# Optimization experiments

Hardware: AMD Instinct MI355X
Metric: run time of the kernel (lower is better)

The kernel has to match this reference:

```python
import jax, jax.numpy as jnp
import numpy as np

N_NODES = 100000
N_EDGES = 1600000
IN_FEATS = 128
N_HIDDEN = 128
N_CLASSES = 47


def _glorot(key, shape):
    fan_in, fan_out = shape
    lim = jnp.sqrt(6.0 / (fan_in + fan_out))
    return jax.random.uniform(key, shape, jnp.float32, -lim, lim)


def setup_inputs() -> dict:
    key = jax.random.key(0)
    ks = jax.random.split(key, 12)
    x = jax.random.normal(ks[0], (N_NODES, IN_FEATS), jnp.float32)
    src = jax.random.randint(ks[1], (N_EDGES,), 0, N_NODES, jnp.int32)
    dst = jax.random.randint(ks[2], (N_EDGES,), 0, N_NODES, jnp.int32)
    dims = [(IN_FEATS, N_HIDDEN), (N_HIDDEN, N_HIDDEN), (N_HIDDEN, N_CLASSES)]
    params = {}
    for l, (di, do) in enumerate(dims):
        params[f"Ws{l}"] = _glorot(ks[3 + 3 * l], (di, do))
        params[f"Wn{l}"] = _glorot(ks[4 + 3 * l], (di, do))
        params[f"b{l}"] = jnp.zeros((do,), jnp.float32)
    return {"x": x, "src": src, "dst": dst, **params}


def _sage_layer(h, src, dst, Ws, Wn, b):
    # mean aggregation over incoming edges (irregular gather + segment-reduce)
    n = h.shape[0]
    msg = h[src]  # [E, F]
    agg = jax.ops.segment_sum(msg, dst, num_segments=n)
    deg = jax.ops.segment_sum(jnp.ones((src.shape[0],), h.dtype), dst, num_segments=n)
    agg = agg / jnp.maximum(deg, 1.0)[:, None]
    return h @ Ws + agg @ Wn + b


def reference(x, src, dst, Ws0, Wn0, b0, Ws1, Wn1, b1, Ws2, Wn2, b2):
    layers = [(Ws0, Wn0, b0), (Ws1, Wn1, b1), (Ws2, Wn2, b2)]
    h = x
    for l, (Ws, Wn, b) in enumerate(layers):
        h = _sage_layer(h, src, dst, Ws, Wn, b)
        if l != len(layers) - 1:
            h = jax.nn.relu(h)  # dropout is identity at inference
    return h
```

## Files before the change

kernel.cpp:

```cpp
#include <hip/hip_runtime.h>
#include <cstdint>
#include <cstddef>

static const int NN = 100000;
static const int NE = 1600000;
static const int F  = 128;
static const int BKT_SHIFT = 9;
static const int BNODES = 1 << BKT_SHIFT;
static const int NBKT = (NN + BNODES - 1) >> BKT_SHIFT;
static const int SRC_BITS = 17;
static const unsigned SRC_MASK = (1u << SRC_BITS) - 1u;

typedef __attribute__((ext_vector_type(8))) short short8;
typedef __attribute__((ext_vector_type(4))) float float4v;
typedef __attribute__((ext_vector_type(2))) float f32x2;

static __device__ __forceinline__ unsigned short f2bf(float f){
    unsigned u = __builtin_bit_cast(unsigned, f);
    unsigned r = (u + 0x7FFFu + ((u >> 16) & 1u)) >> 16;
    return (unsigned short)r;
}
static __device__ __forceinline__ float bf_lo(unsigned u){
    return __builtin_bit_cast(float, u << 16);
}
static __device__ __forceinline__ float bf_hi(unsigned u){
    return __builtin_bit_cast(float, u & 0xFFFF0000u);
}


__global__ __launch_bounds__(256) void bhist_k(const int* __restrict__ dst,
                                               int* __restrict__ bcnt, int E){
    __shared__ int h[NBKT];
    const int t = threadIdx.x;
    for (int i = t; i < NBKT; i += 256) h[i] = 0;
    __syncthreads();
    const int e0 = blockIdx.x * 2048;
    #pragma unroll
    for (int j = 0; j < 8; ++j){
        int e = e0 + j*256 + t;
        if (e < E) atomicAdd(&h[dst[e] >> BKT_SHIFT], 1);
    }
    __syncthreads();
    for (int i = t; i < NBKT; i += 256)
        if (h[i]) atomicAdd(&bcnt[i], h[i]);
}

__global__ __launch_bounds__(256) void bscan_k(const int* __restrict__ bcnt,
                                               int* __restrict__ bptr){
    __shared__ int sm[256];
    int t = threadIdx.x;
    int v = (t < NBKT) ? bcnt[t] : 0;
    sm[t] = v; __syncthreads();
    for (int off = 1; off < 256; off <<= 1){
        int add = (t >= off) ? sm[t-off] : 0;
        __syncthreads();
        sm[t] += add;
        __syncthreads();
    }
    if (t < NBKT) bptr[t+1] = sm[t];
    if (t == 0)   bptr[0] = 0;
}

__global__ __launch_bounds__(256) void bscatter_k(
        const int* __restrict__ src, const int* __restrict__ dst,
        const int* __restrict__ bptr, int* __restrict__ bfill,
        unsigned* __restrict__ pk, int E){
    __shared__ int hist[NBKT];
    __shared__ int gbase[NBKT];
    const int t = threadIdx.x;
    for (int i = t; i < NBKT; i += 256) hist[i] = 0;
    __syncthreads();
    const int e0 = blockIdx.x * 2048;
    int s[8], d[8], b[8], r[8];
    #pragma unroll
    for (int j = 0; j < 8; ++j){
        int e = e0 + j*256 + t;
        if (e < E){
            s[j] = src[e]; d[j] = dst[e];
            b[j] = d[j] >> BKT_SHIFT;
            r[j] = atomicAdd(&hist[b[j]], 1);
        }
    }
    __syncthreads();
    for (int i = t; i < NBKT; i += 256){
        int h = hist[i];
        int base = 0;
        if (h) base = atomicAdd(&bfill[i], h);
        gbase[i] = bptr[i] + base;
    }
    __syncthreads();
    #pragma unroll
    for (int j = 0; j < 8; ++j){
        int e = e0 + j*256 + t;
        if (e < E)
            pk[gbase[b[j]] + r[j]] =
                (unsigned)s[j] | ((unsigned)(d[j] & (BNODES-1)) << SRC_BITS);
    }
}

__global__ __launch_bounds__(1024) void sort_k(
        const unsigned* __restrict__ pk, const int* __restrict__ bptr,
        int* __restrict__ row_ptr, int* __restrict__ ssorted, int N, int E){
    __shared__ int hc[BNODES];
    __shared__ int of[BNODES];
    __shared__ int fi[BNODES];
    const int b  = blockIdx.x;
    const int n0 = b << BKT_SHIFT;
    const int t  = threadIdx.x;
    const int rbeg = bptr[b];
    const int rend = bptr[b+1];
    if (t < BNODES){ hc[t] = 0; fi[t] = 0; }
    __syncthreads();
    for (int e = rbeg + t; e < rend; e += 1024)
        atomicAdd(&hc[pk[e] >> SRC_BITS], 1);
    __syncthreads();
    if (t < BNODES) of[t] = hc[t];
    __syncthreads();
    for (int off = 1; off < BNODES; off <<= 1){
        int add = (t < BNODES && t >= off) ? of[t-off] : 0;
        __syncthreads();
        if (t < BNODES) of[t] += add;
        __syncthreads();
    }
    if (t < BNODES){
        int excl = of[t] - hc[t];
        of[t] = excl;
        int node = n0 + t;
        if (node <= N) row_ptr[node] = rbeg + excl;
    }
    __syncthreads();
    for (int e = rbeg + t; e < rend; e += 1024){
        unsigned p = pk[e];
        int dl = (int)(p >> SRC_BITS);
        int pos = rbeg + of[dl] + atomicAdd(&fi[dl], 1);
        ssorted[pos] = (int)(p & SRC_MASK);
    }
}


__global__ void xconv_k(const float* __restrict__ x, unsigned short* __restrict__ xb, int n4){
    int i = blockIdx.x*256 + threadIdx.x;
    if (i < n4){
        const float4* p = (const float4*)x + i;
        float4 v = *p;
        unsigned short o0 = f2bf(v.x), o1 = f2bf(v.y), o2 = f2bf(v.z), o3 = f2bf(v.w);
        ((unsigned*)xb)[i*2]   = (unsigned)o0 | ((unsigned)o1 << 16);
        ((unsigned*)xb)[i*2+1] = (unsigned)o2 | ((unsigned)o3 << 16);
    }
}

__global__ void prepw_all_k(const float* __restrict__ Ws0, const float* __restrict__ Wn0,
                            const float* __restrict__ Ws1, const float* __restrict__ Wn1,
                            const float* __restrict__ Ws2, const float* __restrict__ Wn2,
                            unsigned short* __restrict__ Wt0, unsigned short* __restrict__ Wt1,
                            unsigned short* __restrict__ Wt2){
    int i = blockIdx.x*256 + threadIdx.x;
    const float* Ws; const float* Wn; unsigned short* Wt; int D; int idx;
    if (i < 32768){       Ws=Ws0; Wn=Wn0; Wt=Wt0; D=128; idx=i; }
    else if (i < 65536){  Ws=Ws1; Wn=Wn1; Wt=Wt1; D=128; idx=i-32768; }
    else {                Ws=Ws2; Wn=Wn2; Wt=Wt2; D=47;  idx=i-65536; }
    int n = idx >> 7, k = idx & 127;
    float v = 0.f;
    if (n < D)        v = Ws[k*D + n];
    else if (n < 2*D) v = Wn[k*D + (n - D)];
    Wt[n*128 + k] = f2bf(v);
}


__global__ __launch_bounds__(256) void gemm_mfma_k(
        const unsigned short* __restrict__ hb,
        const unsigned short* __restrict__ Wt,
        const float* __restrict__ bias,
        unsigned short* __restrict__ Y,
        unsigned short* __restrict__ Z,
        int M, int D, int Dpad){
    __shared__ char ldsA[128*256];
    const int t = threadIdx.x;
    const int lane = t & 63;
    const int w = t >> 6;
    const int wm = w >> 1, wn = w & 1;
    const int tile = blockIdx.x * 128;
    const int cbase = blockIdx.y * 128;

    #pragma unroll
    for (int i = 0; i < 8; ++i){
        int chunkid = i*4 + w;
        int lin = chunkid*64 + lane;
        int row = lin >> 4;
        int cs  = lin & 15;
        int grow = tile + row; if (grow >= M) grow = M - 1;
        const char* src = (const char*)hb + (size_t)grow*256 + ((size_t)(cs ^ (row & 7)) << 4);
        __builtin_amdgcn_global_load_lds(
            (const __attribute__((address_space(1))) void*)src,
            (__attribute__((address_space(3))) void*)(ldsA + (size_t)chunkid*1024 + (size_t)lane*16),
            16, 0, 0);
    }

    short8 bfrag[4][4];
    {
        int ncol = cbase + wn*64;
        #pragma unroll
        for (int n = 0; n < 4; ++n){
            int wrow = ncol + n*16 + (lane & 15);
            const unsigned short* bp = Wt + (size_t)wrow*128 + ((lane >> 4) * 8);
            #pragma unroll
            for (int kk = 0; kk < 4; ++kk)
                bfrag[n][kk] = *(const short8*)(bp + kk*32);
        }
    }

    float4v acc[4][4];
    #pragma unroll
    for (int m = 0; m < 4; ++m)
        #pragma unroll
        for (int n = 0; n < 4; ++n)
            acc[m][n] = (float4v){0.f,0.f,0.f,0.f};

    __syncthreads();

    #pragma unroll
    for (int m = 0; m < 4; ++m){
        int r = wm*64 + m*16 + (lane & 15);
        #pragma unroll
        for (int kk = 0; kk < 4; ++kk){
            int c = kk*4 + (lane >> 4);
            short8 a = *(const short8*)(ldsA + (size_t)r*256 + ((size_t)(c ^ (r & 7)) << 4));
            #pragma unroll
            for (int n = 0; n < 4; ++n)
                acc[m][n] = __builtin_amdgcn_mfma_f32_16x16x32_bf16(a, bfrag[n][kk], acc[m][n], 0, 0, 0);
        }
    }

    #pragma unroll
    for (int m = 0; m < 4; ++m){
        #pragma unroll
        for (int n = 0; n < 4; ++n){
            int c = cbase + wn*64 + n*16 + (lane & 15);
            #pragma unroll
            for (int j = 0; j < 4; ++j){
                int r = tile + wm*64 + m*16 + (lane >> 4)*4 + j;
                if (r < M){
                    float v = acc[m][n][j];
                    if (c < D){
                        v += bias[c];
                        Y[(size_t)r*Dpad + c] = f2bf(v);
                    } else if (c < 2*D){
                        Z[(size_t)r*Dpad + (c - D)] = f2bf(v);
                    }
                }
            }
        }
    }
}


__global__ __launch_bounds__(256) void agg128_k(
        const unsigned short* __restrict__ Yb, const unsigned short* __restrict__ Zb,
        const int* __restrict__ row_ptr, const int* __restrict__ ssorted,
        unsigned short* __restrict__ hout, int N){
    const int lane = threadIdx.x & 63;
    const int q   = lane >> 4;
    const int sub = lane & 15;
    const int node = blockIdx.x*4 + (threadIdx.x >> 6);
    if (node >= N) return;
    const int beg = __builtin_amdgcn_readfirstlane(row_ptr[node]);
    const int end = __builtin_amdgcn_readfirstlane(row_ptr[node+1]);
    const float inv = 1.0f / fmaxf((float)(end - beg), 1.0f);
    const char* zc = (const char*)Zb;
    const unsigned boff = (unsigned)(sub*16);
    f32x2 a0={0.f,0.f}, a1={0.f,0.f}, a2={0.f,0.f}, a3={0.f,0.f};
    for (int e = beg; e < end; e += 32){
        int s[8];
        #pragma unroll
        for (int j = 0; j < 8; ++j){
            int ei = e + 4*j + q;
            int ec = ei < end ? ei : end - 1;
            s[j] = ssorted[ec];
        }
        uint4 u[8];
        #pragma unroll
        for (int j = 0; j < 8; ++j)
            u[j] = *(const uint4*)(zc + ((unsigned)s[j]*256u + boff));
        #pragma unroll
        for (int j = 0; j < 8; ++j){
            if (e + 4*j + q < end){
                a0 += (f32x2){ bf_lo(u[j].x), bf_hi(u[j].x) };
                a1 += (f32x2){ bf_lo(u[j].y), bf_hi(u[j].y) };
                a2 += (f32x2){ bf_lo(u[j].z), bf_hi(u[j].z) };
                a3 += (f32x2){ bf_lo(u[j].w), bf_hi(u[j].w) };
            }
        }
    }
    a0.x += __shfl_xor(a0.x,16,64); a0.x += __shfl_xor(a0.x,32,64);
    a0.y += __shfl_xor(a0.y,16,64); a0.y += __shfl_xor(a0.y,32,64);
    a1.x += __shfl_xor(a1.x,16,64); a1.x += __shfl_xor(a1.x,32,64);
    a1.y += __shfl_xor(a1.y,16,64); a1.y += __shfl_xor(a1.y,32,64);
    a2.x += __shfl_xor(a2.x,16,64); a2.x += __shfl_xor(a2.x,32,64);
    a2.y += __shfl_xor(a2.y,16,64); a2.y += __shfl_xor(a2.y,32,64);
    a3.x += __shfl_xor(a3.x,16,64); a3.x += __shfl_xor(a3.x,32,64);
    a3.y += __shfl_xor(a3.y,16,64); a3.y += __shfl_xor(a3.y,32,64);
    if (q == 0){
        uint4 yu = *(const uint4*)((const char*)Yb + (size_t)node*256 + sub*16);
        float r0 = fmaxf(bf_lo(yu.x) + a0.x*inv, 0.f);
        float r1 = fmaxf(bf_hi(yu.x) + a0.y*inv, 0.f);
        float r2 = fmaxf(bf_lo(yu.y) + a1.x*inv, 0.f);
        float r3 = fmaxf(bf_hi(yu.y) + a1.y*inv, 0.f);
        float r4 = fmaxf(bf_lo(yu.z) + a2.x*inv, 0.f);
        float r5 = fmaxf(bf_hi(yu.z) + a2.y*inv, 0.f);
        float r6 = fmaxf(bf_lo(yu.w) + a3.x*inv, 0.f);
        float r7 = fmaxf(bf_hi(yu.w) + a3.y*inv, 0.f);
        uint4 o;
        o.x = (unsigned)f2bf(r0) | ((unsigned)f2bf(r1) << 16);
        o.y = (unsigned)f2bf(r2) | ((unsigned)f2bf(r3) << 16);
        o.z = (unsigned)f2bf(r4) | ((unsigned)f2bf(r5) << 16);
        o.w = (unsigned)f2bf(r6) | ((unsigned)f2bf(r7) << 16);
        *(uint4*)((char*)hout + (size_t)node*256 + sub*16) = o;
    }
}

__global__ __launch_bounds__(256) void aggfin_k(
        const unsigned short* __restrict__ Yb, const unsigned short* __restrict__ Zb,
        const int* __restrict__ row_ptr, const int* __restrict__ ssorted,
        float* __restrict__ out, int N){
    const int lane = threadIdx.x & 63;
    const int q   = lane >> 4;
    const int sub = lane & 15;
    const int node = blockIdx.x*4 + (threadIdx.x >> 6);
    if (node >= N) return;
    const int beg = __builtin_amdgcn_readfirstlane(row_ptr[node]);
    const int end = __builtin_amdgcn_readfirstlane(row_ptr[node+1]);
    const float inv = 1.0f / fmaxf((float)(end - beg), 1.0f);
    const char* zc = (const char*)Zb;
    const bool act = (sub < 12);
    const unsigned boff = (unsigned)(sub*8);
    f32x2 acc0 = {0.f,0.f}, acc1 = {0.f,0.f};
    for (int e = beg; e < end; e += 32){
        int s[8];
        #pragma unroll
        for (int j = 0; j < 8; ++j){
            int ei = e + 4*j + q;
            int ec = ei < end ? ei : end - 1;
            s[j] = ssorted[ec];
        }
        #pragma unroll
        for (int j = 0; j < 8; ++j){
            if (act){
                uint2 u = *(const uint2*)(zc + ((unsigned)s[j]*96u + boff));
                if (e + 4*j + q < end){
                    acc0 += (f32x2){ bf_lo(u.x), bf_lo(u.y) };
                    acc1 += (f32x2){ bf_hi(u.x), bf_hi(u.y) };
                }
            }
        }
    }
    acc0.x += __shfl_xor(acc0.x, 16, 64); acc0.x += __shfl_xor(acc0.x, 32, 64);
    acc0.y += __shfl_xor(acc0.y, 16, 64); acc0.y += __shfl_xor(acc0.y, 32, 64);
    acc1.x += __shfl_xor(acc1.x, 16, 64); acc1.x += __shfl_xor(acc1.x, 32, 64);
    acc1.y += __shfl_xor(acc1.y, 16, 64); acc1.y += __shfl_xor(acc1.y, 32, 64);
    if (q == 0 && act){
        uint2 yu = *(const uint2*)((const char*)Yb + (size_t)node*96 + sub*8);
        float r0 = bf_lo(yu.x) + acc0.x*inv;
        float r1 = bf_hi(yu.x) + acc1.x*inv;
        float r2 = bf_lo(yu.y) + acc0.y*inv;
        float r3 = bf_hi(yu.y) + acc1.y*inv;
        int f = 4*sub;
        size_t o = (size_t)node*47 + f;
        out[o]   = r0;
        out[o+1] = r1;
        out[o+2] = r2;
        if (f + 3 < 47) out[o+3] = r3;
    }
}


extern "C" void kernel_launch(void* const* d_in, const int* in_sizes, int n_in,
                              void* d_out, int out_size, void* d_ws, size_t ws_size,
                              hipStream_t stream){
    const float* x   = (const float*)d_in[0];
    const int*   src = (const int*)  d_in[1];
    const int*   dstv= (const int*)  d_in[2];
    const float* Ws0 = (const float*)d_in[3];
    const float* Wn0 = (const float*)d_in[4];
    const float* b0  = (const float*)d_in[5];
    const float* Ws1 = (const float*)d_in[6];
    const float* Wn1 = (const float*)d_in[7];
    const float* b1  = (const float*)d_in[8];
    const float* Ws2 = (const float*)d_in[9];
    const float* Wn2 = (const float*)d_in[10];
    const float* b2  = (const float*)d_in[11];
    float* out = (float*)d_out;
    const int N = NN, E = NE;

    char* w = (char*)d_ws;
    size_t off = 0;
    auto alloc = [&](size_t bytes)->char*{
        char* p = w + off; off += (bytes + 255) & ~(size_t)255; return p;
    };
    int*   bbuf    = (int*)  alloc((size_t)(2*NBKT)*4);
    int*   bcnt    = bbuf;
    int*   bfill   = bbuf + NBKT;
    int*   bptr    = (int*)  alloc((size_t)(NBKT+1)*4);
    int*   row_ptr = (int*)  alloc((size_t)(NN+1)*4);
    int*   ssorted = (int*)  alloc((size_t)E*4);
    unsigned* pk   = (unsigned*)alloc((size_t)E*4);
    unsigned short* xb  = (unsigned short*)alloc((size_t)NN*F*2);
    unsigned short* hA  = (unsigned short*)alloc((size_t)NN*F*2);
    unsigned short* hB  = (unsigned short*)alloc((size_t)NN*F*2);
    unsigned short* Yb  = (unsigned short*)alloc((size_t)NN*F*2);
    unsigned short* Zb  = (unsigned short*)alloc((size_t)NN*F*2);
    unsigned short* Wt0 = (unsigned short*)alloc((size_t)256*128*2);
    unsigned short* Wt1 = (unsigned short*)alloc((size_t)256*128*2);
    unsigned short* Wt2 = (unsigned short*)alloc((size_t)128*128*2);
    (void)ws_size; (void)n_in; (void)in_sizes; (void)out_size;

    const int GE = (E + 2047)/2048;

    hipMemsetAsync(bbuf, 0, (size_t)(2*NBKT)*4, stream);
    bhist_k   <<<GE, 256, 0, stream>>>(dstv, bcnt, E);
    bscan_k   <<<1, 256, 0, stream>>>(bcnt, bptr);
    bscatter_k<<<GE, 256, 0, stream>>>(src, dstv, bptr, bfill, pk, E);
    sort_k    <<<NBKT, 1024, 0, stream>>>(pk, bptr, row_ptr, ssorted, N, E);

    xconv_k<<<(N*F/4 + 255)/256, 256, 0, stream>>>(x, xb, N*F/4);
    prepw_all_k<<<320, 256, 0, stream>>>(Ws0, Wn0, Ws1, Wn1, Ws2, Wn2, Wt0, Wt1, Wt2);

    const int GM = (N + 127)/128;
    const int GA = (N + 3)/4;

    gemm_mfma_k<<<dim3(GM,2), 256, 0, stream>>>(xb, Wt0, b0, Yb, Zb, N, 128, 128);
    agg128_k   <<<GA, 256, 0, stream>>>(Yb, Zb, row_ptr, ssorted, hA, N);
    gemm_mfma_k<<<dim3(GM,2), 256, 0, stream>>>(hA, Wt1, b1, Yb, Zb, N, 128, 128);
    agg128_k   <<<GA, 256, 0, stream>>>(Yb, Zb, row_ptr, ssorted, hB, N);
    gemm_mfma_k<<<dim3(GM,1), 256, 0, stream>>>(hB, Wt2, b2, Yb, Zb, N, 47, 48);
    aggfin_k   <<<GA, 256, 0, stream>>>(Yb, Zb, row_ptr, ssorted, out, N);
}
```

Baseline: 388.7 us.

## Drop bucket histogram pass with fixed-capacity buckets; cache edge indices in aggregation

Removes the bucket-count histogram and scan kernels by giving each destination bucket a fixed-capacity slot region (PKCAP) in the packed array. sort_k now recomputes bucket offsets from the fill counters with an in-block scan. The aggregation kernels preload up to 64 source indices per wave and spread them with shuffles instead of reloading them each iteration, and xconv now handles 8 floats per thread. The fixed capacity assumes no bucket gets more than 16384 edges (about 8192 expected for this input), so a skewed dst distribution would overflow silently.

```diff
diff --git a/kernel.cpp b/kernel.cpp
--- a/kernel.cpp
+++ b/kernel.cpp
@@ -8,6 +8,7 @@
 static const int BKT_SHIFT = 9;
 static const int BNODES = 1 << BKT_SHIFT;
 static const int NBKT = (NN + BNODES - 1) >> BKT_SHIFT;
+static const int PKCAP = 16384;
 static const int SRC_BITS = 17;
 static const unsigned SRC_MASK = (1u << SRC_BITS) - 1u;
 
@@ -15,10 +16,9 @@
 typedef __attribute__((ext_vector_type(4))) float float4v;
 typedef __attribute__((ext_vector_type(2))) float f32x2;
 
-static __device__ __forceinline__ unsigned short f2bf(float f){
+static __device__ __forceinline__ unsigned f2bf(float f){
     unsigned u = __builtin_bit_cast(unsigned, f);
-    unsigned r = (u + 0x7FFFu + ((u >> 16) & 1u)) >> 16;
-    return (unsigned short)r;
+    return (u + 0x7FFFu + ((u >> 16) & 1u)) >> 16;
 }
 static __device__ __forceinline__ float bf_lo(unsigned u){
     return __builtin_bit_cast(float, u << 16);
@@ -27,44 +27,9 @@
     return __builtin_bit_cast(float, u & 0xFFFF0000u);
 }
 
-
-__global__ __launch_bounds__(256) void bhist_k(const int* __restrict__ dst,
-                                               int* __restrict__ bcnt, int E){
-    __shared__ int h[NBKT];
-    const int t = threadIdx.x;
-    for (int i = t; i < NBKT; i += 256) h[i] = 0;
-    __syncthreads();
-    const int e0 = blockIdx.x * 2048;
-    #pragma unroll
-    for (int j = 0; j < 8; ++j){
-        int e = e0 + j*256 + t;
-        if (e < E) atomicAdd(&h[dst[e] >> BKT_SHIFT], 1);
-    }
-    __syncthreads();
-    for (int i = t; i < NBKT; i += 256)
-        if (h[i]) atomicAdd(&bcnt[i], h[i]);
-}
-
-__global__ __launch_bounds__(256) void bscan_k(const int* __restrict__ bcnt,
-                                               int* __restrict__ bptr){
-    __shared__ int sm[256];
-    int t = threadIdx.x;
-    int v = (t < NBKT) ? bcnt[t] : 0;
-    sm[t] = v; __syncthreads();
-    for (int off = 1; off < 256; off <<= 1){
-        int add = (t >= off) ? sm[t-off] : 0;
-        __syncthreads();
-        sm[t] += add;
-        __syncthreads();
-    }
-    if (t < NBKT) bptr[t+1] = sm[t];
-    if (t == 0)   bptr[0] = 0;
-}
-
 __global__ __launch_bounds__(256) void bscatter_k(
         const int* __restrict__ src, const int* __restrict__ dst,
-        const int* __restrict__ bptr, int* __restrict__ bfill,
-        unsigned* __restrict__ pk, int E){
+        int* __restrict__ bfill, unsigned* __restrict__ pk, int E){
     __shared__ int hist[NBKT];
     __shared__ int gbase[NBKT];
     const int t = threadIdx.x;
@@ -86,7 +51,7 @@
         int h = hist[i];
         int base = 0;
         if (h) base = atomicAdd(&bfill[i], h);
-        gbase[i] = bptr[i] + base;
+        gbase[i] = i*PKCAP + base;
     }
     __syncthreads();
     #pragma unroll
@@ -99,20 +64,28 @@
 }
 
 __global__ __launch_bounds__(1024) void sort_k(
-        const unsigned* __restrict__ pk, const int* __restrict__ bptr,
-        int* __restrict__ row_ptr, int* __restrict__ ssorted, int N, int E){
+        const unsigned* __restrict__ pk, const int* __restrict__ bfill,
+        int* __restrict__ row_ptr, int* __restrict__ ssorted, int N){
+    __shared__ int bs[256];
     __shared__ int hc[BNODES];
     __shared__ int of[BNODES];
     __shared__ int fi[BNODES];
-    const int b  = blockIdx.x;
-    const int n0 = b << BKT_SHIFT;
-    const int t  = threadIdx.x;
-    const int rbeg = bptr[b];
-    const int rend = bptr[b+1];
+    const int b = blockIdx.x;
+    const int t = threadIdx.x;
+    if (t < 256) bs[t] = (t < NBKT) ? bfill[t] : 0;
     if (t < BNODES){ hc[t] = 0; fi[t] = 0; }
     __syncthreads();
-    for (int e = rbeg + t; e < rend; e += 1024)
-        atomicAdd(&hc[pk[e] >> SRC_BITS], 1);
+    for (int off = 1; off < 256; off <<= 1){
+        int add = (t < 256 && t >= off) ? bs[t-off] : 0;
+        __syncthreads();
+        if (t < 256) bs[t] += add;
+        __syncthreads();
+    }
+    const int cntb = bfill[b];
+    const int rbeg = bs[b] - cntb;
+    const unsigned* mypk = pk + (size_t)b * PKCAP;
+    for (int i = t; i < cntb; i += 1024)
+        atomicAdd(&hc[mypk[i] >> SRC_BITS], 1);
     __syncthreads();
     if (t < BNODES) of[t] = hc[t];
     __syncthreads();
@@ -125,12 +98,13 @@
     if (t < BNODES){
         int excl = of[t] - hc[t];
         of[t] = excl;
-        int node = n0 + t;
-        if (node <= N) row_ptr[node] = rbeg + excl;
-    }
-    __syncthreads();
-    for (int e = rbeg + t; e < rend; e += 1024){
-        unsigned p = pk[e];
+        int node = (b << BKT_SHIFT) + t;
+        if (node < N) row_ptr[node] = rbeg + excl;
+    }
+    if (b == 0 && t == 0) row_ptr[N] = NE;
+    __syncthreads();
+    for (int i = t; i < cntb; i += 1024){
+        unsigned p = mypk[i];
         int dl = (int)(p >> SRC_BITS);
         int pos = rbeg + of[dl] + atomicAdd(&fi[dl], 1);
         ssorted[pos] = (int)(p & SRC_MASK);
@@ -138,14 +112,17 @@
 }
 
 
-__global__ void xconv_k(const float* __restrict__ x, unsigned short* __restrict__ xb, int n4){
+__global__ void xconv_k(const float* __restrict__ x, unsigned short* __restrict__ xb, int n8){
     int i = blockIdx.x*256 + threadIdx.x;
-    if (i < n4){
-        const float4* p = (const float4*)x + i;
-        float4 v = *p;
-        unsigned short o0 = f2bf(v.x), o1 = f2bf(v.y), o2 = f2bf(v.z), o3 = f2bf(v.w);
-        ((unsigned*)xb)[i*2]   = (unsigned)o0 | ((unsigned)o1 << 16);
-        ((unsigned*)xb)[i*2+1] = (unsigned)o2 | ((unsigned)o3 << 16);
+    if (i < n8){
+        float4 v0 = ((const float4*)x)[i*2];
+        float4 v1 = ((const float4*)x)[i*2+1];
+        uint4 o;
+        o.x = f2bf(v0.x) | (f2bf(v0.y) << 16);
+        o.y = f2bf(v0.z) | (f2bf(v0.w) << 16);
+        o.z = f2bf(v1.x) | (f2bf(v1.y) << 16);
+        o.w = f2bf(v1.z) | (f2bf(v1.w) << 16);
+        ((uint4*)xb)[i] = o;
     }
 }
 
@@ -163,7 +140,7 @@
     float v = 0.f;
     if (n < D)        v = Ws[k*D + n];
     else if (n < 2*D) v = Wn[k*D + (n - D)];
-    Wt[n*128 + k] = f2bf(v);
+    Wt[n*128 + k] = (unsigned short)f2bf(v);
 }
 
 
@@ -243,9 +220,9 @@
                     float v = acc[m][n][j];
                     if (c < D){
                         v += bias[c];
-                        Y[(size_t)r*Dpad + c] = f2bf(v);
+                        Y[(size_t)r*Dpad + c] = (unsigned short)f2bf(v);
                     } else if (c < 2*D){
-                        Z[(size_t)r*Dpad + (c - D)] = f2bf(v);
+                        Z[(size_t)r*Dpad + (c - D)] = (unsigned short)f2bf(v);
                     }
                 }
             }
@@ -268,19 +245,27 @@
     const float inv = 1.0f / fmaxf((float)(end - beg), 1.0f);
     const char* zc = (const char*)Zb;
     const unsigned boff = (unsigned)(sub*16);
+    int ecache;
+    { int ei0 = beg + lane; if (ei0 > NE-1) ei0 = NE-1; ecache = ssorted[ei0]; }
     f32x2 a0={0.f,0.f}, a1={0.f,0.f}, a2={0.f,0.f}, a3={0.f,0.f};
     for (int e = beg; e < end; e += 32){
-        int s[8];
+        int rel0 = e - beg;
+        int sidx[8];
+        #pragma unroll
+        for (int j = 0; j < 8; ++j){
+            int rel = rel0 + 4*j + q;
+            sidx[j] = __shfl(ecache, rel & 63, 64);
+        }
+        uint4 u[8];
         #pragma unroll
         for (int j = 0; j < 8; ++j){
             int ei = e + 4*j + q;
-            int ec = ei < end ? ei : end - 1;
-            s[j] = ssorted[ec];
-        }
-        uint4 u[8];
-        #pragma unroll
-        for (int j = 0; j < 8; ++j)
-            u[j] = *(const uint4*)(zc + ((unsigned)s[j]*256u + boff));
+            if (ei < end){
+                int rel = rel0 + 4*j + q;
+                int s = (rel < 64) ? sidx[j] : ssorted[ei];
+                u[j] = *(const uint4*)(zc + ((unsigned)s*256u + boff));
+            }
+        }
         #pragma unroll
         for (int j = 0; j < 8; ++j){
             if (e + 4*j + q < end){
@@ -310,10 +295,10 @@
         float r6 = fmaxf(bf_lo(yu.w) + a3.x*inv, 0.f);
         float r7 = fmaxf(bf_hi(yu.w) + a3.y*inv, 0.f);
         uint4 o;
-        o.x = (unsigned)f2bf(r0) | ((unsigned)f2bf(r1) << 16);
-        o.y = (unsigned)f2bf(r2) | ((unsigned)f2bf(r3) << 16);
-        o.z = (unsigned)f2bf(r4) | ((unsigned)f2bf(r5) << 16);
-        o.w = (unsigned)f2bf(r6) | ((unsigned)f2bf(r7) << 16);
+        o.x = f2bf(r0) | (f2bf(r1) << 16);
+        o.y = f2bf(r2) | (f2bf(r3) << 16);
+        o.z = f2bf(r4) | (f2bf(r5) << 16);
+        o.w = f2bf(r6) | (f2bf(r7) << 16);
         *(uint4*)((char*)hout + (size_t)node*256 + sub*16) = o;
     }
 }
@@ -333,23 +318,32 @@
     const char* zc = (const char*)Zb;
     const bool act = (sub < 12);
     const unsigned boff = (unsigned)(sub*8);
+    int ecache;
+    { int ei0 = beg + lane; if (ei0 > NE-1) ei0 = NE-1; ecache = ssorted[ei0]; }
     f32x2 acc0 = {0.f,0.f}, acc1 = {0.f,0.f};
     for (int e = beg; e < end; e += 32){
-        int s[8];
+        int rel0 = e - beg;
+        int sidx[8];
+        #pragma unroll
+        for (int j = 0; j < 8; ++j){
+            int rel = rel0 + 4*j + q;
+            sidx[j] = __shfl(ecache, rel & 63, 64);
+        }
+        uint2 u[8];
         #pragma unroll
         for (int j = 0; j < 8; ++j){
             int ei = e + 4*j + q;
-            int ec = ei < end ? ei : end - 1;
-            s[j] = ssorted[ec];
-        }
-        #pragma unroll
-        for (int j = 0; j < 8; ++j){
-            if (act){
-                uint2 u = *(const uint2*)(zc + ((unsigned)s[j]*96u + boff));
-                if (e + 4*j + q < end){
-                    acc0 += (f32x2){ bf_lo(u.x), bf_lo(u.y) };
-                    acc1 += (f32x2){ bf_hi(u.x), bf_hi(u.y) };
-                }
+            if (act && ei < end){
+                int rel = rel0 + 4*j + q;
+                int s = (rel < 64) ? sidx[j] : ssorted[ei];
+                u[j] = *(const uint2*)(zc + ((unsigned)s*96u + boff));
+            }
+        }
+        #pragma unroll
+        for (int j = 0; j < 8; ++j){
+            if (act && e + 4*j + q < end){
+                acc0 += (f32x2){ bf_lo(u[j].x), bf_lo(u[j].y) };
+                acc1 += (f32x2){ bf_hi(u[j].x), bf_hi(u[j].y) };
             }
         }
     }
@@ -396,13 +390,10 @@
     auto alloc = [&](size_t bytes)->char*{
         char* p = w + off; off += (bytes + 255) & ~(size_t)255; return p;
     };
-    int*   bbuf    = (int*)  alloc((size_t)(2*NBKT)*4);
-    int*   bcnt    = bbuf;
-    int*   bfill   = bbuf + NBKT;
-    int*   bptr    = (int*)  alloc((size_t)(NBKT+1)*4);
+    int*   bfill   = (int*)  alloc((size_t)NBKT*4);
     int*   row_ptr = (int*)  alloc((size_t)(NN+1)*4);
     int*   ssorted = (int*)  alloc((size_t)E*4);
-    unsigned* pk   = (unsigned*)alloc((size_t)E*4);
+    unsigned* pk   = (unsigned*)alloc((size_t)NBKT*PKCAP*4);
     unsigned short* xb  = (unsigned short*)alloc((size_t)NN*F*2);
     unsigned short* hA  = (unsigned short*)alloc((size_t)NN*F*2);
     unsigned short* hB  = (unsigned short*)alloc((size_t)NN*F*2);
@@ -415,13 +406,11 @@
 
     const int GE = (E + 2047)/2048;
 
-    hipMemsetAsync(bbuf, 0, (size_t)(2*NBKT)*4, stream);
-    bhist_k   <<<GE, 256, 0, stream>>>(dstv, bcnt, E);
-    bscan_k   <<<1, 256, 0, stream>>>(bcnt, bptr);
-    bscatter_k<<<GE, 256, 0, stream>>>(src, dstv, bptr, bfill, pk, E);
-    sort_k    <<<NBKT, 1024, 0, stream>>>(pk, bptr, row_ptr, ssorted, N, E);
-
-    xconv_k<<<(N*F/4 + 255)/256, 256, 0, stream>>>(x, xb, N*F/4);
+    hipMemsetAsync(bfill, 0, (size_t)NBKT*4, stream);
+    bscatter_k<<<GE, 256, 0, stream>>>(src, dstv, bfill, pk, E);
+    sort_k    <<<NBKT, 1024, 0, stream>>>(pk, bfill, row_ptr, ssorted, N);
+
+    xconv_k<<<(N*F/8 + 255)/256, 256, 0, stream>>>(x, xb, N*F/8);
     prepw_all_k<<<320, 256, 0, stream>>>(Ws0, Wn0, Ws1, Wn1, Ws2, Wn2, Wt0, Wt1, Wt2);
 
     const int GM = (N + 127)/128;
```

After: 375.3 us. -3.5%, faster.
